# Kernel tuning notes

Hardware: AMD Instinct MI355X
Metric: run time of the kernel (lower is better)

## Reference

```python
import jax, jax.numpy as jnp
import numpy as np

# Static tree: complete 8-ary tree, depth 3 (breadth-first numbering).
BRANCH = 8
LEVEL_SIZES = [1, 8, 64, 512]            # levels 0..3, total 585 nodes
LEVEL_STARTS = [0, 1, 9, 73]
N_NODES = 585
IN_DIM, MEM_DIM, BATCH = 512, 256, 256


def setup_inputs() -> dict:
    key = jax.random.key(0)
    ks = jax.random.split(key, 10)
    s_in = 1.0 / np.sqrt(IN_DIM)
    s_m = 1.0 / np.sqrt(MEM_DIM)
    return {
        "inputs": jax.random.normal(ks[0], (N_NODES, BATCH, IN_DIM), jnp.float32),
        "prob": jax.random.uniform(ks[1], (N_NODES, N_NODES), jnp.float32),
        "Wioux": jax.random.uniform(ks[2], (3 * MEM_DIM, IN_DIM), jnp.float32, -s_in, s_in),
        "bioux": jax.random.uniform(ks[3], (3 * MEM_DIM,), jnp.float32, -s_in, s_in),
        "Wiouh": jax.random.uniform(ks[4], (3 * MEM_DIM, MEM_DIM), jnp.float32, -s_m, s_m),
        "biouh": jax.random.uniform(ks[5], (3 * MEM_DIM,), jnp.float32, -s_m, s_m),
        "Wfx": jax.random.uniform(ks[6], (MEM_DIM, IN_DIM), jnp.float32, -s_in, s_in),
        "bfx": jax.random.uniform(ks[7], (MEM_DIM,), jnp.float32, -s_in, s_in),
        "Wfh": jax.random.uniform(ks[8], (MEM_DIM, MEM_DIM), jnp.float32, -s_m, s_m),
        "bfh": jax.random.uniform(ks[9], (MEM_DIM,), jnp.float32, -s_m, s_m),
    }


def _node_forward(x, child_c, child_h, Wioux, bioux, Wiouh, biouh, Wfx, bfx, Wfh, bfh):
    # x: (L,B,D); child_c/child_h: (L,K,B,M). Batched over all nodes of a level.
    child_h_sum = child_h.sum(axis=1)                               # (L,B,M)
    iou = x @ Wioux.T + bioux + child_h_sum @ Wiouh.T + biouh      # (L,B,3M)
    i, o, u = jnp.split(iou, 3, axis=-1)
    i, o, u = jax.nn.sigmoid(i), jax.nn.sigmoid(o), jnp.tanh(u)
    fx = (x @ Wfx.T + bfx)[:, None]                                # (L,1,B,M)
    f = jax.nn.sigmoid(child_h @ Wfh.T + bfh + fx)                 # (L,K,B,M)
    c = i * u + (f * child_c).sum(axis=1)                          # (L,B,M)
    h = o * jnp.tanh(c)
    return c, h


def reference(inputs, prob, Wioux, bioux, Wiouh, biouh, Wfx, bfx, Wfh, bfh):
    B, M = inputs.shape[1], MEM_DIM
    c_all = jnp.zeros((N_NODES, B, M), inputs.dtype)
    h_all = jnp.zeros((N_NODES, B, M), inputs.dtype)
    n_levels = len(LEVEL_SIZES)
    for level in reversed(range(n_levels)):
        s, L = LEVEL_STARTS[level], LEVEL_SIZES[level]
        x = inputs[s:s + L]
        if level == n_levels - 1:
            # leaves: single zero child (matches original leaf path)
            child_c = jnp.zeros((L, 1, B, M), inputs.dtype)
            child_h = jnp.zeros((L, 1, B, M), inputs.dtype)
        else:
            nodes = np.arange(s, s + L)
            children = nodes[:, None] * BRANCH + np.arange(1, BRANCH + 1)  # (L,K) static
            w = prob[nodes[:, None], children][:, :, None, None]           # (L,K,1,1)
            child_c = c_all[children] * w
            child_h = h_all[children] * w
        c, h = _node_forward(x, child_c, child_h, Wioux, bioux, Wiouh, biouh,
                             Wfx, bfx, Wfh, bfh)
        c_all = c_all.at[s:s + L].set(c)
        h_all = h_all.at[s:s + L].set(h)
    return h_all  # bottom-up hidden state for every node: (N, batch, mem_dim)
```

## Files before the change

kernel.cpp:

```cpp
#include <hip/hip_runtime.h>
#include <math.h>

typedef _Float16 h8_t __attribute__((ext_vector_type(8)));
typedef _Float16 h4_t __attribute__((ext_vector_type(4)));
typedef float f4_t __attribute__((ext_vector_type(4)));


__device__ __forceinline__ float fsig(float x) {
  return __builtin_amdgcn_rcpf(1.f + __expf(-x));
}
__device__ __forceinline__ float ftanh(float x) {
  float e = __expf(-2.f * fabsf(x));
  float t = (1.f - e) * __builtin_amdgcn_rcpf(1.f + e);
  return copysignf(t, x);
}

__device__ __forceinline__ int xcd_swz_lin(int lin, int nwg) {
  if (nwg & 7) return lin;
  int cpx = nwg >> 3;
  return (lin & 7) * cpx + (lin >> 3);
}

__device__ __forceinline__ void gload16(const _Float16* g, _Float16* l) {
  __builtin_amdgcn_global_load_lds(
      (const __attribute__((address_space(1))) void*)g,
      (__attribute__((address_space(3))) void*)l, 16, 0, 0);
}

template <int R>
__device__ __forceinline__ void gstage(const _Float16* __restrict__ src, int ld,
                                       _Float16* __restrict__ dst, int t) {
#pragma unroll
  for (int it = 0; it < R / 64; ++it) {
    int idx = t + it * 256;
    int row = idx >> 2;
    int kq  = (idx & 3) << 3;
    gload16(src + (size_t)row * ld + kq, dst + (size_t)idx * 8);
  }
}

template <int R>
__device__ __forceinline__ void loadA_f32(const float* __restrict__ src, int ld,
                                          int t, float4* v) {
#pragma unroll
  for (int it = 0; it < R / 32; ++it) {
    int idx = t + it * 256;
    int row = idx >> 3;
    int kg  = (idx & 7) << 2;
    v[it] = *(const float4*)(src + (size_t)row * ld + kg);
  }
}
template <int R>
__device__ __forceinline__ void writeA_f16(_Float16* __restrict__ dst, int t,
                                           const float4* v) {
#pragma unroll
  for (int it = 0; it < R / 32; ++it) {
    int idx = t + it * 256;
    int row = idx >> 3;
    int kg  = (idx & 7) << 2;
    h4_t h = {(_Float16)v[it].x, (_Float16)v[it].y,
              (_Float16)v[it].z, (_Float16)v[it].w};
    *(h4_t*)(dst + row * 32 + kg) = h;
  }
}

__global__ __launch_bounds__(256) void convert_weights(
    const float* __restrict__ Wioux, const float* __restrict__ Wiouh,
    const float* __restrict__ Wfx, const float* __restrict__ Wfh,
    _Float16* __restrict__ Wx, _Float16* __restrict__ Wh,
    _Float16* __restrict__ Wfxh, _Float16* __restrict__ Wfhh)
{
  int i4 = (blockIdx.x * 256 + threadIdx.x) * 4;
  const float* src; _Float16* dst; int off;
  if (i4 < 393216)      { src = Wioux; dst = Wx;   off = i4; }
  else if (i4 < 589824) { src = Wiouh; dst = Wh;   off = i4 - 393216; }
  else if (i4 < 720896) { src = Wfx;   dst = Wfxh; off = i4 - 589824; }
  else                  { src = Wfh;   dst = Wfhh; off = i4 - 720896; }
  float4 v = *(const float4*)(src + off);
  h4_t h = {(_Float16)v.x, (_Float16)v.y, (_Float16)v.z, (_Float16)v.w};
  *(h4_t*)(dst + off) = h;
}

__global__ __launch_bounds__(256) void fx_gemm(
    const float* __restrict__ x, const _Float16* __restrict__ Wfx,
    float* __restrict__ out)
{
  __shared__ _Float16 As[64 * 32];
  __shared__ _Float16 Bs[256 * 32];
  const int t = threadIdx.x;
  int swz = xcd_swz_lin(blockIdx.x, gridDim.x);
  const int r0 = swz * 64;
  const int w = t >> 6, lane = t & 63;
  const int wr = (w >> 1) * 32, wc = (w & 1) * 128;
  const int fr = lane & 15, fq = (lane >> 4) * 8;
  f4_t acc[2][8] = {};
  float4 va[2], vn[2];
  loadA_f32<64>(x + (size_t)r0 * 512, 512, t, va);
  for (int k0 = 0; k0 < 512; k0 += 32) {
    __syncthreads();
    writeA_f16<64>(As, t, va);
    gstage<256>(Wfx + (size_t)k0, 512, Bs, t);
    __syncthreads();
    if (k0 + 32 < 512)
      loadA_f32<64>(x + (size_t)r0 * 512 + k0 + 32, 512, t, vn);
    h8_t a[2], b[8];
#pragma unroll
    for (int rt = 0; rt < 2; ++rt)
      a[rt] = *(const h8_t*)(As + (wr + rt * 16 + fr) * 32 + fq);
#pragma unroll
    for (int ct = 0; ct < 8; ++ct)
      b[ct] = *(const h8_t*)(Bs + (wc + ct * 16 + fr) * 32 + fq);
#pragma unroll
    for (int rt = 0; rt < 2; ++rt)
#pragma unroll
      for (int ct = 0; ct < 8; ++ct)
        acc[rt][ct] = __builtin_amdgcn_mfma_f32_16x16x32_f16(a[rt], b[ct], acc[rt][ct], 0, 0, 0);
    if (k0 + 32 < 512) { va[0] = vn[0]; va[1] = vn[1]; }
  }
#pragma unroll
  for (int rt = 0; rt < 2; ++rt)
#pragma unroll
    for (int ct = 0; ct < 8; ++ct)
#pragma unroll
      for (int i = 0; i < 4; ++i) {
        int row = wr + rt * 16 + (lane >> 4) * 4 + i;
        int col = wc + ct * 16 + (lane & 15);
        out[(size_t)(r0 + row) * 256 + col] = acc[rt][ct][i];
      }
}

__global__ __launch_bounds__(256) void fh_gemm(
    const float* __restrict__ h_src, const _Float16* __restrict__ Wfh,
    _Float16* __restrict__ out)
{
  __shared__ _Float16 As[64 * 32];
  __shared__ _Float16 Bs[256 * 32];
  const int t = threadIdx.x;
  int swz = xcd_swz_lin(blockIdx.x, gridDim.x);
  const int r0 = swz * 64;
  const int w = t >> 6, lane = t & 63;
  const int wr = (w >> 1) * 32, wc = (w & 1) * 128;
  const int fr = lane & 15, fq = (lane >> 4) * 8;
  f4_t acc[2][8] = {};
  float4 va[2], vn[2];
  loadA_f32<64>(h_src + (size_t)r0 * 256, 256, t, va);
  for (int k0 = 0; k0 < 256; k0 += 32) {
    __syncthreads();
    writeA_f16<64>(As, t, va);
    gstage<256>(Wfh + (size_t)k0, 256, Bs, t);
    __syncthreads();
    if (k0 + 32 < 256)
      loadA_f32<64>(h_src + (size_t)r0 * 256 + k0 + 32, 256, t, vn);
    h8_t a[2], b[8];
#pragma unroll
    for (int rt = 0; rt < 2; ++rt)
      a[rt] = *(const h8_t*)(As + (wr + rt * 16 + fr) * 32 + fq);
#pragma unroll
    for (int ct = 0; ct < 8; ++ct)
      b[ct] = *(const h8_t*)(Bs + (wc + ct * 16 + fr) * 32 + fq);
#pragma unroll
    for (int rt = 0; rt < 2; ++rt)
#pragma unroll
      for (int ct = 0; ct < 8; ++ct)
        acc[rt][ct] = __builtin_amdgcn_mfma_f32_16x16x32_f16(a[rt], b[ct], acc[rt][ct], 0, 0, 0);
    if (k0 + 32 < 256) { va[0] = vn[0]; va[1] = vn[1]; }
  }
#pragma unroll
  for (int rt = 0; rt < 2; ++rt)
#pragma unroll
    for (int ct = 0; ct < 8; ++ct)
#pragma unroll
      for (int i = 0; i < 4; ++i) {
        int row = wr + rt * 16 + (lane >> 4) * 4 + i;
        int col = wc + ct * 16 + (lane & 15);
        out[(size_t)(r0 + row) * 256 + col] = (_Float16)acc[rt][ct][i];
      }
}

__global__ __launch_bounds__(256) void chs_fgate(
    const float* __restrict__ h_all, const _Float16* __restrict__ fh,
    const _Float16* __restrict__ c_half, const float* __restrict__ prob,
    const float* __restrict__ bfh, const float* __restrict__ bfx,
    const float* __restrict__ fxb, _Float16* __restrict__ chs,
    float* __restrict__ cacc, int s, int cs)
{
  int blk = xcd_swz_lin(blockIdx.x, gridDim.x);
  int idx = blk * 256 + threadIdx.x;
  int m = (idx & 63) << 2;
  int b = (idx >> 6) & 255;
  int nl = idx >> 14;
  int node = s + nl;
  float4 vfx = *(const float4*)(fxb + ((size_t)node * 256 + b) * 256 + m);
  float4 vbh = *(const float4*)(bfh + m);
  float4 vbx = *(const float4*)(bfx + m);
  float b0 = vfx.x + vbh.x + vbx.x;
  float b1 = vfx.y + vbh.y + vbx.y;
  float b2 = vfx.z + vbh.z + vbx.z;
  float b3 = vfx.w + vbh.w + vbx.w;
  float4 hacc = {0.f, 0.f, 0.f, 0.f};
  float4 cc = {0.f, 0.f, 0.f, 0.f};
#pragma unroll
  for (int j = 0; j < 8; ++j) {
    int child = node * 8 + 1 + j;
    float wv = prob[node * 585 + child];
    float4 hv = *(const float4*)(h_all + (size_t)child * 65536 + b * 256 + m);
    hacc.x += wv * hv.x; hacc.y += wv * hv.y;
    hacc.z += wv * hv.z; hacc.w += wv * hv.w;
    h4_t fv = *(const h4_t*)(fh + (size_t)(child - cs) * 65536 + b * 256 + m);
    h4_t cv = *(const h4_t*)(c_half + (size_t)child * 65536 + b * 256 + m);
    cc.x += wv * (float)cv[0] * fsig(wv * (float)fv[0] + b0);
    cc.y += wv * (float)cv[1] * fsig(wv * (float)fv[1] + b1);
    cc.z += wv * (float)cv[2] * fsig(wv * (float)fv[2] + b2);
    cc.w += wv * (float)cv[3] * fsig(wv * (float)fv[3] + b3);
  }
  h4_t hc = {(_Float16)hacc.x, (_Float16)hacc.y, (_Float16)hacc.z, (_Float16)hacc.w};
  *(h4_t*)(chs + (size_t)nl * 65536 + b * 256 + m) = hc;
  *(float4*)(cacc + ((size_t)nl * 256 + b) * 256 + m) = cc;
}

template <int CT>
__global__ __launch_bounds__(256) void iou_fused(
    const float* __restrict__ x, const _Float16* __restrict__ chs,
    const float* __restrict__ cacc,
    const _Float16* __restrict__ Wx, const _Float16* __restrict__ Wh,
    const float* __restrict__ bioux, const float* __restrict__ biouh,
    _Float16* __restrict__ c_half, float* __restrict__ h_all, int node0)
{
  __shared__ _Float16 As[64 * 32];
  __shared__ _Float16 Bs[3][CT * 32 * 32];
  const int t = threadIdx.x;
  int swz = xcd_swz_lin(blockIdx.y * gridDim.x + blockIdx.x,
                        gridDim.x * gridDim.y);
  const int m0 = (swz % gridDim.x) * (CT * 32);
  const int r0 = (swz / gridDim.x) * 64;
  const int w = t >> 6, lane = t & 63;
  const int wr = (w >> 1) * 32, wc = (w & 1) * (CT * 16);
  const int fr = lane & 15, fq = (lane >> 4) * 8;

  f4_t acc[3][2][CT] = {};
  for (int ph = 0; ph < 2; ++ph) {
    if (ph == 1 && chs == nullptr) break;
    const int K = ph ? 256 : 512;
    const _Float16* W = ph ? Wh : Wx;
    float4 va[2], vn[2];
    if (ph == 0) loadA_f32<64>(x + (size_t)r0 * 512, 512, t, va);
    for (int k0 = 0; k0 < K; k0 += 32) {
      __syncthreads();
      if (ph == 0) writeA_f16<64>(As, t, va);
      else         gstage<64>(chs + (size_t)r0 * 256 + k0, 256, As, t);
#pragma unroll
      for (int g = 0; g < 3; ++g)
        gstage<CT * 32>(W + (size_t)(g * 256 + m0) * K + k0, K, &Bs[g][0], t);
      __syncthreads();
      if (ph == 0 && k0 + 32 < K)
        loadA_f32<64>(x + (size_t)r0 * 512 + k0 + 32, 512, t, vn);
      h8_t a[2], b[3][CT];
#pragma unroll
      for (int rt = 0; rt < 2; ++rt)
        a[rt] = *(const h8_t*)(As + (wr + rt * 16 + fr) * 32 + fq);
#pragma unroll
      for (int g = 0; g < 3; ++g)
#pragma unroll
        for (int ct = 0; ct < CT; ++ct)
          b[g][ct] = *(const h8_t*)(&Bs[g][0] + (wc + ct * 16 + fr) * 32 + fq);
#pragma unroll
      for (int g = 0; g < 3; ++g)
#pragma unroll
        for (int rt = 0; rt < 2; ++rt)
#pragma unroll
          for (int ct = 0; ct < CT; ++ct)
            acc[g][rt][ct] = __builtin_amdgcn_mfma_f32_16x16x32_f16(a[rt], b[g][ct], acc[g][rt][ct], 0, 0, 0);
      if (ph == 0 && k0 + 32 < K) { va[0] = vn[0]; va[1] = vn[1]; }
    }
  }
#pragma unroll
  for (int rt = 0; rt < 2; ++rt)
#pragma unroll
    for (int ct = 0; ct < CT; ++ct)
#pragma unroll
      for (int i = 0; i < 4; ++i) {
        int row = wr + rt * 16 + (lane >> 4) * 4 + i;
        int col = wc + ct * 16 + (lane & 15);
        int m = m0 + col;
        size_t lrow = (size_t)(r0 + row);
        float iv = acc[0][rt][ct][i] + bioux[m] + biouh[m];
        float ov = acc[1][rt][ct][i] + bioux[256 + m] + biouh[256 + m];
        float uv = acc[2][rt][ct][i] + bioux[512 + m] + biouh[512 + m];
        float c = fsig(iv) * ftanh(uv) + (cacc ? cacc[lrow * 256 + m] : 0.f);
        float h = fsig(ov) * ftanh(c);
        size_t g = ((size_t)node0 * 256 + lrow) * 256 + m;
        h_all[g] = h;
        c_half[g] = (_Float16)c;
      }
}

extern "C" void kernel_launch(void* const* d_in, const int* in_sizes, int n_in,
                              void* d_out, int out_size, void* d_ws, size_t ws_size,
                              hipStream_t stream) {
  const float* inputs = (const float*)d_in[0];
  const float* prob   = (const float*)d_in[1];
  const float* Wioux  = (const float*)d_in[2];
  const float* bioux  = (const float*)d_in[3];
  const float* Wiouh  = (const float*)d_in[4];
  const float* biouh  = (const float*)d_in[5];
  const float* Wfx    = (const float*)d_in[6];
  const float* bfx    = (const float*)d_in[7];
  const float* Wfh    = (const float*)d_in[8];
  const float* bfh    = (const float*)d_in[9];
  float* h_out = (float*)d_out;

  char* p = (char*)d_ws;
  _Float16* c_half = (_Float16*)p; p += (size_t)585 * 65536 * 2;
  _Float16* fh     = (_Float16*)p; p += (size_t)512 * 65536 * 2;
  float*    fxb    = (float*)p;    p += (size_t)73 * 65536 * 4;
  _Float16* chs    = (_Float16*)p; p += (size_t)64 * 65536 * 2;
  float*    cacc   = (float*)p;    p += (size_t)64 * 65536 * 4;
  _Float16* Wx     = (_Float16*)p; p += (size_t)393216 * 2;
  _Float16* Wh     = (_Float16*)p; p += (size_t)196608 * 2;
  _Float16* Wfxh   = (_Float16*)p; p += (size_t)131072 * 2;
  _Float16* Wfhh   = (_Float16*)p; p += (size_t)65536 * 2;

  convert_weights<<<768, 256, 0, stream>>>(Wioux, Wiouh, Wfx, Wfh, Wx, Wh, Wfxh, Wfhh);
  fx_gemm<<<292, 256, 0, stream>>>(inputs, Wfxh, fxb);

  iou_fused<4><<<dim3(2, 2048), 256, 0, stream>>>(
      inputs + (size_t)73 * 131072, nullptr, nullptr,
      Wx, Wh, bioux, biouh, c_half, h_out, 73);
  fh_gemm<<<2048, 256, 0, stream>>>(
      h_out + (size_t)73 * 65536, Wfhh, fh);

  chs_fgate<<<64 * 64, 256, 0, stream>>>(
      h_out, fh, c_half, prob, bfh, bfx, fxb, chs, cacc, 9, 73);
  iou_fused<4><<<dim3(2, 256), 256, 0, stream>>>(
      inputs + (size_t)9 * 131072, chs, cacc,
      Wx, Wh, bioux, biouh, c_half, h_out, 9);
  fh_gemm<<<256, 256, 0, stream>>>(
      h_out + (size_t)9 * 65536, Wfhh, fh);

  chs_fgate<<<8 * 64, 256, 0, stream>>>(
      h_out, fh, c_half, prob, bfh, bfx, fxb, chs, cacc, 1, 9);
  iou_fused<2><<<dim3(4, 32), 256, 0, stream>>>(
      inputs + (size_t)1 * 131072, chs, cacc,
      Wx, Wh, bioux, biouh, c_half, h_out, 1);
  fh_gemm<<<32, 256, 0, stream>>>(
      h_out + (size_t)1 * 65536, Wfhh, fh);

  chs_fgate<<<64, 256, 0, stream>>>(
      h_out, fh, c_half, prob, bfh, bfx, fxb, chs, cacc, 0, 1);
  iou_fused<2><<<dim3(4, 4), 256, 0, stream>>>(
      inputs, chs, cacc,
      Wx, Wh, bioux, biouh, c_half, h_out, 0);
}
```

Measured before the change: 853.2 us.

## Double-buffer LDS tiles and XOR-swizzle layout in GEMM kernels

Converts the fx, fh and iou GEMM main loops to double-buffered LDS, prefetching the next K-slice into the alternate buffer while MFMAs run on the current one. This drops one barrier per iteration. It also adds an XOR swizzle on the 16-byte chunk index for both staged and register-written tiles, aiming to reduce LDS bank conflicts on the h8 fragment reads. LDS usage per block doubles, which may lower occupancy. The cur buffer index carries across the two phases of iou_fused.

```diff
diff --git a/kernel.cpp b/kernel.cpp
--- a/kernel.cpp
+++ b/kernel.cpp
@@ -5,6 +5,10 @@
 typedef _Float16 h4_t __attribute__((ext_vector_type(4)));
 typedef float f4_t __attribute__((ext_vector_type(4)));
 
+
+__device__ __forceinline__ int swz(int row, int fq) {
+  return fq ^ (((row >> 1) & 3) << 3);
+}
 
 __device__ __forceinline__ float fsig(float x) {
   return __builtin_amdgcn_rcpf(1.f + __expf(-x));
@@ -34,7 +38,8 @@
   for (int it = 0; it < R / 64; ++it) {
     int idx = t + it * 256;
     int row = idx >> 2;
-    int kq  = (idx & 3) << 3;
+    int sl  = idx & 3;
+    int kq  = (sl ^ ((row >> 1) & 3)) << 3;
     gload16(src + (size_t)row * ld + kq, dst + (size_t)idx * 8);
   }
 }
@@ -57,10 +62,12 @@
   for (int it = 0; it < R / 32; ++it) {
     int idx = t + it * 256;
     int row = idx >> 3;
-    int kg  = (idx & 7) << 2;
-    h4_t h = {(_Float16)v[it].x, (_Float16)v[it].y,
-              (_Float16)v[it].z, (_Float16)v[it].w};
-    *(h4_t*)(dst + row * 32 + kg) = h;
+    int c   = idx & 7;
+    int g   = c >> 1, h = c & 1;
+    int sl  = g ^ ((row >> 1) & 3);
+    h4_t hv = {(_Float16)v[it].x, (_Float16)v[it].y,
+               (_Float16)v[it].z, (_Float16)v[it].w};
+    *(h4_t*)(dst + row * 32 + sl * 8 + h * 4) = hv;
   }
 }
 
@@ -85,37 +92,48 @@
     const float* __restrict__ x, const _Float16* __restrict__ Wfx,
     float* __restrict__ out)
 {
-  __shared__ _Float16 As[64 * 32];
-  __shared__ _Float16 Bs[256 * 32];
+  __shared__ _Float16 As[2][64 * 32];
+  __shared__ _Float16 Bs[2][256 * 32];
   const int t = threadIdx.x;
-  int swz = xcd_swz_lin(blockIdx.x, gridDim.x);
-  const int r0 = swz * 64;
+  int swzb = xcd_swz_lin(blockIdx.x, gridDim.x);
+  const int r0 = swzb * 64;
   const int w = t >> 6, lane = t & 63;
   const int wr = (w >> 1) * 32, wc = (w & 1) * 128;
   const int fr = lane & 15, fq = (lane >> 4) * 8;
   f4_t acc[2][8] = {};
-  float4 va[2], vn[2];
+  float4 va[2];
   loadA_f32<64>(x + (size_t)r0 * 512, 512, t, va);
+  writeA_f16<64>(As[0], t, va);
+  gstage<256>(Wfx, 512, Bs[0], t);
+  loadA_f32<64>(x + (size_t)r0 * 512 + 32, 512, t, va);
+  __syncthreads();
+  int cur = 0;
   for (int k0 = 0; k0 < 512; k0 += 32) {
-    __syncthreads();
-    writeA_f16<64>(As, t, va);
-    gstage<256>(Wfx + (size_t)k0, 512, Bs, t);
-    __syncthreads();
-    if (k0 + 32 < 512)
-      loadA_f32<64>(x + (size_t)r0 * 512 + k0 + 32, 512, t, vn);
+    int nxt = cur ^ 1;
+    if (k0 + 32 < 512) {
+      writeA_f16<64>(As[nxt], t, va);
+      gstage<256>(Wfx + (size_t)(k0 + 32), 512, Bs[nxt], t);
+      if (k0 + 64 < 512)
+        loadA_f32<64>(x + (size_t)r0 * 512 + k0 + 64, 512, t, va);
+    }
     h8_t a[2], b[8];
 #pragma unroll
-    for (int rt = 0; rt < 2; ++rt)
-      a[rt] = *(const h8_t*)(As + (wr + rt * 16 + fr) * 32 + fq);
-#pragma unroll
-    for (int ct = 0; ct < 8; ++ct)
-      b[ct] = *(const h8_t*)(Bs + (wc + ct * 16 + fr) * 32 + fq);
+    for (int rt = 0; rt < 2; ++rt) {
+      int row = wr + rt * 16 + fr;
+      a[rt] = *(const h8_t*)(As[cur] + row * 32 + swz(row, fq));
+    }
+#pragma unroll
+    for (int ct = 0; ct < 8; ++ct) {
+      int row = wc + ct * 16 + fr;
+      b[ct] = *(const h8_t*)(Bs[cur] + row * 32 + swz(row, fq));
+    }
 #pragma unroll
     for (int rt = 0; rt < 2; ++rt)
 #pragma unroll
       for (int ct = 0; ct < 8; ++ct)
         acc[rt][ct] = __builtin_amdgcn_mfma_f32_16x16x32_f16(a[rt], b[ct], acc[rt][ct], 0, 0, 0);
-    if (k0 + 32 < 512) { va[0] = vn[0]; va[1] = vn[1]; }
+    __syncthreads();
+    cur = nxt;
   }
 #pragma unroll
   for (int rt = 0; rt < 2; ++rt)
@@ -133,37 +151,48 @@
     const float* __restrict__ h_src, const _Float16* __restrict__ Wfh,
     _Float16* __restrict__ out)
 {
-  __shared__ _Float16 As[64 * 32];
-  __shared__ _Float16 Bs[256 * 32];
+  __shared__ _Float16 As[2][64 * 32];
+  __shared__ _Float16 Bs[2][256 * 32];
   const int t = threadIdx.x;
-  int swz = xcd_swz_lin(blockIdx.x, gridDim.x);
-  const int r0 = swz * 64;
+  int swzb = xcd_swz_lin(blockIdx.x, gridDim.x);
+  const int r0 = swzb * 64;
   const int w = t >> 6, lane = t & 63;
   const int wr = (w >> 1) * 32, wc = (w & 1) * 128;
   const int fr = lane & 15, fq = (lane >> 4) * 8;
   f4_t acc[2][8] = {};
-  float4 va[2], vn[2];
+  float4 va[2];
   loadA_f32<64>(h_src + (size_t)r0 * 256, 256, t, va);
+  writeA_f16<64>(As[0], t, va);
+  gstage<256>(Wfh, 256, Bs[0], t);
+  loadA_f32<64>(h_src + (size_t)r0 * 256 + 32, 256, t, va);
+  __syncthreads();
+  int cur = 0;
   for (int k0 = 0; k0 < 256; k0 += 32) {
-    __syncthreads();
-    writeA_f16<64>(As, t, va);
-    gstage<256>(Wfh + (size_t)k0, 256, Bs, t);
-    __syncthreads();
-    if (k0 + 32 < 256)
-      loadA_f32<64>(h_src + (size_t)r0 * 256 + k0 + 32, 256, t, vn);
+    int nxt = cur ^ 1;
+    if (k0 + 32 < 256) {
+      writeA_f16<64>(As[nxt], t, va);
+      gstage<256>(Wfh + (size_t)(k0 + 32), 256, Bs[nxt], t);
+      if (k0 + 64 < 256)
+        loadA_f32<64>(h_src + (size_t)r0 * 256 + k0 + 64, 256, t, va);
+    }
     h8_t a[2], b[8];
 #pragma unroll
-    for (int rt = 0; rt < 2; ++rt)
-      a[rt] = *(const h8_t*)(As + (wr + rt * 16 + fr) * 32 + fq);
-#pragma unroll
-    for (int ct = 0; ct < 8; ++ct)
-      b[ct] = *(const h8_t*)(Bs + (wc + ct * 16 + fr) * 32 + fq);
+    for (int rt = 0; rt < 2; ++rt) {
+      int row = wr + rt * 16 + fr;
+      a[rt] = *(const h8_t*)(As[cur] + row * 32 + swz(row, fq));
+    }
+#pragma unroll
+    for (int ct = 0; ct < 8; ++ct) {
+      int row = wc + ct * 16 + fr;
+      b[ct] = *(const h8_t*)(Bs[cur] + row * 32 + swz(row, fq));
+    }
 #pragma unroll
     for (int rt = 0; rt < 2; ++rt)
 #pragma unroll
       for (int ct = 0; ct < 8; ++ct)
         acc[rt][ct] = __builtin_amdgcn_mfma_f32_16x16x32_f16(a[rt], b[ct], acc[rt][ct], 0, 0, 0);
-    if (k0 + 32 < 256) { va[0] = vn[0]; va[1] = vn[1]; }
+    __syncthreads();
+    cur = nxt;
   }
 #pragma unroll
   for (int rt = 0; rt < 2; ++rt)
@@ -226,43 +255,62 @@
     const float* __restrict__ bioux, const float* __restrict__ biouh,
     _Float16* __restrict__ c_half, float* __restrict__ h_all, int node0)
 {
-  __shared__ _Float16 As[64 * 32];
-  __shared__ _Float16 Bs[3][CT * 32 * 32];
+  __shared__ _Float16 As[2][64 * 32];
+  __shared__ _Float16 Bs[2][3][CT * 32 * 32];
   const int t = threadIdx.x;
-  int swz = xcd_swz_lin(blockIdx.y * gridDim.x + blockIdx.x,
-                        gridDim.x * gridDim.y);
-  const int m0 = (swz % gridDim.x) * (CT * 32);
-  const int r0 = (swz / gridDim.x) * 64;
+  int swzb = xcd_swz_lin(blockIdx.y * gridDim.x + blockIdx.x,
+                         gridDim.x * gridDim.y);
+  const int m0 = (swzb % gridDim.x) * (CT * 32);
+  const int r0 = (swzb / gridDim.x) * 64;
   const int w = t >> 6, lane = t & 63;
   const int wr = (w >> 1) * 32, wc = (w & 1) * (CT * 16);
   const int fr = lane & 15, fq = (lane >> 4) * 8;
 
   f4_t acc[3][2][CT] = {};
+  int cur = 0;
   for (int ph = 0; ph < 2; ++ph) {
     if (ph == 1 && chs == nullptr) break;
     const int K = ph ? 256 : 512;
     const _Float16* W = ph ? Wh : Wx;
-    float4 va[2], vn[2];
-    if (ph == 0) loadA_f32<64>(x + (size_t)r0 * 512, 512, t, va);
+    float4 va[2];
+    if (ph == 0) {
+      loadA_f32<64>(x + (size_t)r0 * 512, 512, t, va);
+      writeA_f16<64>(As[cur], t, va);
+    } else {
+      gstage<64>(chs + (size_t)r0 * 256, 256, As[cur], t);
+    }
+#pragma unroll
+    for (int g = 0; g < 3; ++g)
+      gstage<CT * 32>(W + (size_t)(g * 256 + m0) * K, K, &Bs[cur][g][0], t);
+    if (ph == 0)
+      loadA_f32<64>(x + (size_t)r0 * 512 + 32, 512, t, va);
+    __syncthreads();
+
     for (int k0 = 0; k0 < K; k0 += 32) {
-      __syncthreads();
-      if (ph == 0) writeA_f16<64>(As, t, va);
-      else         gstage<64>(chs + (size_t)r0 * 256 + k0, 256, As, t);
+      int nxt = cur ^ 1;
+      if (k0 + 32 < K) {
+        if (ph == 0) writeA_f16<64>(As[nxt], t, va);
+        else gstage<64>(chs + (size_t)r0 * 256 + k0 + 32, 256, As[nxt], t);
+#pragma unroll
+        for (int g = 0; g < 3; ++g)
+          gstage<CT * 32>(W + (size_t)(g * 256 + m0) * K + k0 + 32, K,
+                          &Bs[nxt][g][0], t);
+        if (ph == 0 && k0 + 64 < K)
+          loadA_f32<64>(x + (size_t)r0 * 512 + k0 + 64, 512, t, va);
+      }
+      h8_t a[2], b[3][CT];
+#pragma unroll
+      for (int rt = 0; rt < 2; ++rt) {
+        int row = wr + rt * 16 + fr;
+        a[rt] = *(const h8_t*)(As[cur] + row * 32 + swz(row, fq));
+      }
 #pragma unroll
       for (int g = 0; g < 3; ++g)
-        gstage<CT * 32>(W + (size_t)(g * 256 + m0) * K + k0, K, &Bs[g][0], t);
-      __syncthreads();
-      if (ph == 0 && k0 + 32 < K)
-        loadA_f32<64>(x + (size_t)r0 * 512 + k0 + 32, 512, t, vn);
-      h8_t a[2], b[3][CT];
-#pragma unroll
-      for (int rt = 0; rt < 2; ++rt)
-        a[rt] = *(const h8_t*)(As + (wr + rt * 16 + fr) * 32 + fq);
-#pragma unroll
-      for (int g = 0; g < 3; ++g)
-#pragma unroll
-        for (int ct = 0; ct < CT; ++ct)
-          b[g][ct] = *(const h8_t*)(&Bs[g][0] + (wc + ct * 16 + fr) * 32 + fq);
+#pragma unroll
+        for (int ct = 0; ct < CT; ++ct) {
+          int row = wc + ct * 16 + fr;
+          b[g][ct] = *(const h8_t*)(&Bs[cur][g][0] + row * 32 + swz(row, fq));
+        }
 #pragma unroll
       for (int g = 0; g < 3; ++g)
 #pragma unroll
@@ -270,7 +318,8 @@
 #pragma unroll
           for (int ct = 0; ct < CT; ++ct)
             acc[g][rt][ct] = __builtin_amdgcn_mfma_f32_16x16x32_f16(a[rt], b[g][ct], acc[g][rt][ct], 0, 0, 0);
-      if (ph == 0 && k0 + 32 < K) { va[0] = vn[0]; va[1] = vn[1]; }
+      __syncthreads();
+      cur = nxt;
     }
   }
 #pragma unroll
```

After: 1.016 ms. 1.19x slower.
